# Kernel optimization log

Hardware: AMD Instinct MI355X
Metric: run time of the kernel (lower is better)

Reference implementation:

```python
import jax, jax.numpy as jnp
import numpy as np

B, S, D, H = 2, 2048, 1024, 16


def setup_inputs() -> dict:
    key = jax.random.key(0)
    kq, kk, kv1, kv2 = jax.random.split(key, 4)
    return {
        "q": jax.random.normal(kq, (B, S, D), dtype=jnp.float32),
        "k": jax.random.normal(kk, (B, S, D), dtype=jnp.float32),
        "v1": jax.random.normal(kv1, (B, S, D), dtype=jnp.float32),
        "v2": jax.random.normal(kv2, (B, S, D), dtype=jnp.float32),
        "num_attn_heads": 16,
    }


def _split_heads(x, h):
    b, s, d = x.shape
    return x.reshape(b, s, h, d // h).transpose(0, 2, 1, 3)  # [B,H,S,dh]


def reference(q, k, v1, v2, num_attn_heads):
    h = num_attn_heads
    b, s, d = q.shape
    dh = d // h
    qh = _split_heads(q, h)
    kh = _split_heads(k, h)
    v1h = _split_heads(v1, h)
    v2h = _split_heads(v2, h)
    scores = jnp.einsum("bhqd,bhkd->bhqk", qh, kh) / jnp.sqrt(jnp.float32(dh))
    # Faithful to create_mask(input, 0): nopeek = triu(ones, k=0); mask = (nopeek == 0)
    # -> only STRICTLY lower triangle is visible; diagonal and above get -1e9.
    # Row 0 is fully masked -> softmax uniform (same as torch behavior).
    allowed = jnp.tril(jnp.ones((s, s), dtype=bool), k=-1)  # [S,S] j < i
    scores = jnp.where(allowed[None, None], scores, jnp.float32(-1e9))
    p_attn = jax.nn.softmax(scores, axis=-1)  # dropout p=0.0 -> identity
    o1 = jnp.einsum("bhqk,bhkd->bhqd", p_attn, v1h)
    o2 = jnp.einsum("bhqk,bhkd->bhqd", p_attn, v2h)
    o1 = o1.transpose(0, 2, 1, 3).reshape(b, s, d)
    o2 = o2.transpose(0, 2, 1, 3).reshape(b, s, d)
    return (o1, o2)
```

## Files before the change

### kernel.cpp

```cpp
#include <hip/hip_runtime.h>

#define B_ 2
#define S_ 2048
#define D_ 1024
#define H_ 16
#define DH 64
#define OFF2 (B_ * S_ * D_)

typedef __attribute__((ext_vector_type(8))) __bf16 bf16x8;
typedef __attribute__((ext_vector_type(4))) float f32x4;
typedef __attribute__((ext_vector_type(4))) unsigned int u32x4;
typedef __attribute__((address_space(3))) unsigned int lds_u32;
typedef __attribute__((address_space(1))) const unsigned int glob_u32;

__device__ __forceinline__ unsigned short f2bf(float f) {
    return __builtin_bit_cast(unsigned short, (__bf16)f);
}
__device__ __forceinline__ float bf2f(unsigned short h) {
    unsigned int u = ((unsigned int)h) << 16;
    return __builtin_bit_cast(float, u);
}

template <int CTRL>
__device__ __forceinline__ float dpp_ror(float x) {
    return __builtin_bit_cast(float, __builtin_amdgcn_update_dpp(
        0, __builtin_bit_cast(int, x), CTRL, 0xf, 0xf, false));
}
__device__ __forceinline__ float rowsum16(float x) {
    x += dpp_ror<0x121>(x);
    x += dpp_ror<0x122>(x);
    x += dpp_ror<0x124>(x);
    x += dpp_ror<0x128>(x);
    return x;
}

__global__ void prep_all(const float* __restrict__ q, const float* __restrict__ k,
                         const float* __restrict__ v1, const float* __restrict__ v2,
                         unsigned short* __restrict__ qb, unsigned short* __restrict__ kb,
                         unsigned short* __restrict__ v1t, unsigned short* __restrict__ v2t) {
    int id = blockIdx.x;
    if (id < 4096) {
        int ysel = id & 1;
        int cid = (id >> 1) * 256 + threadIdx.x;
        const float* src = ysel ? k : q;
        unsigned short* dst = ysel ? kb : qb;
        float scale = ysel ? 1.0f : 0.125f * 1.4426950408889634f;
        int d8 = cid & 7;
        int s  = (cid >> 3) & (S_ - 1);
        int h  = (cid >> 14) & (H_ - 1);
        int b  = cid >> 18;
        int off = (b * S_ + s) * D_ + h * DH + d8 * 8;
        float4 f0 = *(const float4*)(src + off);
        float4 f1 = *(const float4*)(src + off + 4);
        unsigned int w0 = f2bf(f0.x * scale) | ((unsigned int)f2bf(f0.y * scale) << 16);
        unsigned int w1 = f2bf(f0.z * scale) | ((unsigned int)f2bf(f0.w * scale) << 16);
        unsigned int w2 = f2bf(f1.x * scale) | ((unsigned int)f2bf(f1.y * scale) << 16);
        unsigned int w3 = f2bf(f1.z * scale) | ((unsigned int)f2bf(f1.w * scale) << 16);
        u32x4 wv = {w0, w1, w2, w3};
        *(u32x4*)(dst + cid * 8) = wv;
        return;
    }
    __shared__ __align__(16) unsigned short ldsT[64][72];
    int id2 = id - 4096;
    int t = threadIdx.x;
    int s0 = (id2 & 31) * 64;
    int bh = (id2 >> 5) & 31;
    int b = bh >> 4, h = bh & 15;
    const float* src = (id2 >> 10) ? v2 : v1;
    unsigned short* dst = (id2 >> 10) ? v2t : v1t;
    {
        int sl = t >> 2, dc = t & 3;
        int off = (b * S_ + s0 + sl) * D_ + h * DH + dc * 16;
#pragma unroll
        for (int i4 = 0; i4 < 4; i4++) {
            float4 f = *(const float4*)(src + off + i4 * 4);
            int d = dc * 16 + i4 * 4;
            ldsT[d + 0][sl] = f2bf(f.x);
            ldsT[d + 1][sl] = f2bf(f.y);
            ldsT[d + 2][sl] = f2bf(f.z);
            ldsT[d + 3][sl] = f2bf(f.w);
        }
    }
    __syncthreads();
    {
        int d = t >> 2, sc = t & 3;
        u32x4 a = *(const u32x4*)(&ldsT[d][sc * 16]);
        u32x4 c = *(const u32x4*)(&ldsT[d][sc * 16 + 8]);
        int off = (bh * DH + d) * S_ + s0 + sc * 16;
        *(u32x4*)(dst + off) = a;
        *(u32x4*)(dst + off + 8) = c;
    }
}

__global__ __launch_bounds__(256) void flash_attn(
        const unsigned short* __restrict__ qb, const unsigned short* __restrict__ kb,
        const unsigned short* __restrict__ v1t, const unsigned short* __restrict__ v2t,
        float* __restrict__ out) {
    __shared__ __align__(16) unsigned short sK0[4096], sK1[4096];
    __shared__ __align__(16) unsigned short sV1[4096], sV2[4096];
    __shared__ __align__(16) unsigned short sP[4][1024];

    int tid = threadIdx.x;
    int w = tid >> 6, lane = tid & 63;
    int lr = lane & 15, lg = lane >> 4;

    int id = blockIdx.x;
    int xcd = id & 7;
    int j = id >> 3;
    int bh = xcd * 4 + (j & 3);
    int qt = 31 - (j >> 2);

    const unsigned short* gK  = kb  + bh * (S_ * DH);
    const unsigned short* gV1 = v1t + bh * (DH * S_);
    const unsigned short* gV2 = v2t + bh * (DH * S_);
    unsigned short* sPw = sP[w];

    int srow = tid >> 3, sco = tid & 7;

    auto stageV = [&](int t) {
#pragma unroll
        for (int jj = 0; jj < 2; jj++) {
            int row = srow + jj * 32;
            int cosw = (sco ^ (row & 7)) * 8;
            int c8 = (tid + jj * 256) * 8;
            __builtin_amdgcn_global_load_lds((glob_u32*)(gV1 + row * S_ + t * 64 + cosw),
                                             (lds_u32*)(sV1 + c8), 16, 0, 0);
            __builtin_amdgcn_global_load_lds((glob_u32*)(gV2 + row * S_ + t * 64 + cosw),
                                             (lds_u32*)(sV2 + c8), 16, 0, 0);
        }
    };
    auto stageK = [&](unsigned short* dK, int t) {
#pragma unroll
        for (int jj = 0; jj < 2; jj++) {
            int row = srow + jj * 32;
            int cosw = (sco ^ (row & 7)) * 8;
            int c8 = (tid + jj * 256) * 8;
            __builtin_amdgcn_global_load_lds((glob_u32*)(gK + (t * 64 + row) * 64 + cosw),
                                             (lds_u32*)(dK + c8), 16, 0, 0);
        }
    };

    bf16x8 qa[2];
    {
        int qoff = (bh * S_ + qt * 64 + w * 16 + lr) * DH + lg * 8;
        qa[0] = __builtin_bit_cast(bf16x8, *(const u32x4*)(qb + qoff));
        qa[1] = __builtin_bit_cast(bf16x8, *(const u32x4*)(qb + qoff + 32));
    }

    f32x4 acc1[4], acc2[4];
    float l[4];
#pragma unroll
    for (int dt = 0; dt < 4; dt++) {
        acc1[dt] = (f32x4){0.f, 0.f, 0.f, 0.f};
        acc2[dt] = (f32x4){0.f, 0.f, 0.f, 0.f};
    }
#pragma unroll
    for (int r = 0; r < 4; r++) l[r] = 0.f;

    stageK(sK0, 0);
    asm volatile("s_waitcnt vmcnt(0)" ::: "memory");
    __builtin_amdgcn_s_barrier();

    for (int t = 0; t <= qt; t++) {
        const unsigned short* cK = (t & 1) ? sK1 : sK0;
        unsigned short* nK       = (t & 1) ? sK0 : sK1;
        stageV(t);
        int tn = (t < qt) ? (t + 1) : qt;
        stageK(nK, tn);
        f32x4 s[4];
        __builtin_amdgcn_s_setprio(1);
#pragma unroll
        for (int n = 0; n < 4; n++) {
            f32x4 accs = (f32x4){0.f, 0.f, 0.f, 0.f};
#pragma unroll
            for (int ks = 0; ks < 2; ks++) {
                int kv = n * 16 + lr;
                int idx = ((kv << 6) + ks * 32 + lg * 8) ^ ((kv & 7) << 3);
                bf16x8 bk = __builtin_bit_cast(bf16x8, *(const u32x4*)(cK + idx));
                accs = __builtin_amdgcn_mfma_f32_16x16x32_bf16(qa[ks], bk, accs, 0, 0, 0);
            }
            s[n] = accs;
        }
        __builtin_amdgcn_s_setprio(0);
        if (t == qt) {
#pragma unroll
            for (int n = 0; n < 4; n++) {
                int kv = n * 16 + lr;
#pragma unroll
                for (int r = 0; r < 4; r++) {
                    int qrow = w * 16 + lg * 4 + r;
                    if (kv >= qrow) s[n][r] = -1e30f;
                }
            }
        }
#pragma unroll
        for (int n = 0; n < 4; n++)
#pragma unroll
            for (int r = 0; r < 4; r++) {
                float pv = __builtin_amdgcn_exp2f(s[n][r] - 20.0f);
                l[r] += pv;
                int rowp = lg * 4 + r, col = n * 16 + lr;
                sPw[((rowp << 6) + col) ^ ((rowp & 7) << 3)] = f2bf(pv);
            }
        asm volatile("s_waitcnt lgkmcnt(0)" ::: "memory");
        asm volatile("s_waitcnt vmcnt(2)" ::: "memory");
        __builtin_amdgcn_s_barrier();
        __builtin_amdgcn_s_setprio(1);
#pragma unroll
        for (int ks = 0; ks < 2; ks++) {
            int pidx = ((lr << 6) + ks * 32 + lg * 8) ^ ((lr & 7) << 3);
            bf16x8 ap = __builtin_bit_cast(bf16x8, *(const u32x4*)(sPw + pidx));
#pragma unroll
            for (int dt = 0; dt < 4; dt++) {
                int d = dt * 16 + lr;
                int vidx = ((d << 6) + ks * 32 + lg * 8) ^ ((d & 7) << 3);
                bf16x8 bv1 = __builtin_bit_cast(bf16x8, *(const u32x4*)(sV1 + vidx));
                acc1[dt] = __builtin_amdgcn_mfma_f32_16x16x32_bf16(ap, bv1, acc1[dt], 0, 0, 0);
                bf16x8 bv2 = __builtin_bit_cast(bf16x8, *(const u32x4*)(sV2 + vidx));
                acc2[dt] = __builtin_amdgcn_mfma_f32_16x16x32_bf16(ap, bv2, acc2[dt], 0, 0, 0);
            }
        }
        __builtin_amdgcn_s_setprio(0);
        asm volatile("s_waitcnt vmcnt(0)" ::: "memory");
        __builtin_amdgcn_s_barrier();
    }

    {
        int b = bh >> 4, h = bh & 15;
#pragma unroll
        for (int r = 0; r < 4; r++) {
            float lsum = rowsum16(l[r]);
            float inv = 1.0f / lsum;
            int qrow = qt * 64 + w * 16 + lg * 4 + r;
            int base = (b * S_ + qrow) * D_ + h * DH + lr;
#pragma unroll
            for (int dt = 0; dt < 4; dt++) {
                out[base + dt * 16] = acc1[dt][r] * inv;
                out[base + dt * 16 + OFF2] = acc2[dt][r] * inv;
            }
        }
    }
}

__global__ void row0_mean(const unsigned short* __restrict__ v1t,
                          const unsigned short* __restrict__ v2t,
                          float* __restrict__ out) {
    int wid = blockIdx.x * 4 + (threadIdx.x >> 6);
    int lane = threadIdx.x & 63;
    int tz = wid >> 11;
    int bhd = wid & 2047;
    const unsigned short* src = (tz ? v2t : v1t) + bhd * S_;
    float sum = 0.f;
#pragma unroll
    for (int kk = 0; kk < 4; kk++) {
        u32x4 v = *(const u32x4*)(src + (kk * 64 + lane) * 8);
#pragma unroll
        for (int jj = 0; jj < 4; jj++) {
            unsigned int u = v[jj];
            sum += bf2f((unsigned short)(u & 0xffff)) + bf2f((unsigned short)(u >> 16));
        }
    }
#pragma unroll
    for (int msk = 32; msk >= 1; msk >>= 1) sum += __shfl_xor(sum, msk, 64);
    if (lane == 0) {
        int b = bhd >> 10, rem = bhd & 1023, h = rem >> 6, d = rem & 63;
        out[tz * OFF2 + b * (S_ * D_) + h * DH + d] = sum * (1.0f / S_);
    }
}

extern "C" void kernel_launch(void* const* d_in, const int* in_sizes, int n_in,
                              void* d_out, int out_size, void* d_ws, size_t ws_size,
                              hipStream_t stream) {
    const float* q  = (const float*)d_in[0];
    const float* k  = (const float*)d_in[1];
    const float* v1 = (const float*)d_in[2];
    const float* v2 = (const float*)d_in[3];
    float* out = (float*)d_out;

    const int ELEMS = B_ * H_ * S_ * DH;
    unsigned short* qb  = (unsigned short*)d_ws;
    unsigned short* kb  = qb + ELEMS;
    unsigned short* v1t = kb + ELEMS;
    unsigned short* v2t = v1t + ELEMS;

    prep_all<<<6144, 256, 0, stream>>>(q, k, v1, v2, qb, kb, v1t, v2t);
    flash_attn<<<1024, 256, 0, stream>>>(qb, kb, v1t, v2t, out);
    row0_mean<<<1024, 256, 0, stream>>>(v1t, v2t, out);
}
```

Measured before the change: 76.63 us.

## Split PV matmul across waves by output tensor and row half via shared P tile

P is now written to a single block-wide shared tile instead of per-wave tiles. Each wave computes PV for one value tensor (V1 or V2) over 32 query rows, rather than both tensors over its own 16 rows. The end-of-iteration wait and barrier move to the start of the next iteration so the next tile's loads overlap more with compute. Row sums are reduced through LDS so each wave can normalize rows it did not compute. The intent is to halve V fragment LDS reads per wave and to remove a barrier per iteration, at the cost of extra P reads and tighter vmcnt accounting.

```diff
diff --git a/kernel.cpp b/kernel.cpp
--- a/kernel.cpp
+++ b/kernel.cpp
@@ -98,7 +98,7 @@
         float* __restrict__ out) {
     __shared__ __align__(16) unsigned short sK0[4096], sK1[4096];
     __shared__ __align__(16) unsigned short sV1[4096], sV2[4096];
-    __shared__ __align__(16) unsigned short sP[4][1024];
+    __shared__ __align__(16) unsigned short sP[4096];
 
     int tid = threadIdx.x;
     int w = tid >> 6, lane = tid & 63;
@@ -113,7 +113,6 @@
     const unsigned short* gK  = kb  + bh * (S_ * DH);
     const unsigned short* gV1 = v1t + bh * (DH * S_);
     const unsigned short* gV2 = v2t + bh * (DH * S_);
-    unsigned short* sPw = sP[w];
 
     int srow = tid >> 3, sco = tid & 7;
 
@@ -147,26 +146,27 @@
         qa[1] = __builtin_bit_cast(bf16x8, *(const u32x4*)(qb + qoff + 32));
     }
 
-    f32x4 acc1[4], acc2[4];
+    int tz = w >> 1, half = w & 1;
+    const unsigned short* cV = tz ? sV2 : sV1;
+
+    f32x4 acc[2][4];
     float l[4];
 #pragma unroll
-    for (int dt = 0; dt < 4; dt++) {
-        acc1[dt] = (f32x4){0.f, 0.f, 0.f, 0.f};
-        acc2[dt] = (f32x4){0.f, 0.f, 0.f, 0.f};
-    }
+    for (int m = 0; m < 2; m++)
+#pragma unroll
+        for (int dt = 0; dt < 4; dt++) acc[m][dt] = (f32x4){0.f, 0.f, 0.f, 0.f};
 #pragma unroll
     for (int r = 0; r < 4; r++) l[r] = 0.f;
 
     stageK(sK0, 0);
-    asm volatile("s_waitcnt vmcnt(0)" ::: "memory");
-    __builtin_amdgcn_s_barrier();
 
     for (int t = 0; t <= qt; t++) {
         const unsigned short* cK = (t & 1) ? sK1 : sK0;
         unsigned short* nK       = (t & 1) ? sK0 : sK1;
+        __builtin_amdgcn_s_barrier();
         stageV(t);
-        int tn = (t < qt) ? (t + 1) : qt;
-        stageK(nK, tn);
+        stageK(nK, (t < qt) ? t + 1 : qt);
+        asm volatile("s_waitcnt vmcnt(6)" ::: "memory");
         f32x4 s[4];
         __builtin_amdgcn_s_setprio(1);
 #pragma unroll
@@ -199,46 +199,56 @@
             for (int r = 0; r < 4; r++) {
                 float pv = __builtin_amdgcn_exp2f(s[n][r] - 20.0f);
                 l[r] += pv;
-                int rowp = lg * 4 + r, col = n * 16 + lr;
-                sPw[((rowp << 6) + col) ^ ((rowp & 7) << 3)] = f2bf(pv);
+                int row = w * 16 + lg * 4 + r, col = n * 16 + lr;
+                sP[((row << 6) + col) ^ ((row & 7) << 3)] = f2bf(pv);
             }
         asm volatile("s_waitcnt lgkmcnt(0)" ::: "memory");
         asm volatile("s_waitcnt vmcnt(2)" ::: "memory");
         __builtin_amdgcn_s_barrier();
         __builtin_amdgcn_s_setprio(1);
 #pragma unroll
-        for (int ks = 0; ks < 2; ks++) {
-            int pidx = ((lr << 6) + ks * 32 + lg * 8) ^ ((lr & 7) << 3);
-            bf16x8 ap = __builtin_bit_cast(bf16x8, *(const u32x4*)(sPw + pidx));
-#pragma unroll
-            for (int dt = 0; dt < 4; dt++) {
-                int d = dt * 16 + lr;
-                int vidx = ((d << 6) + ks * 32 + lg * 8) ^ ((d & 7) << 3);
-                bf16x8 bv1 = __builtin_bit_cast(bf16x8, *(const u32x4*)(sV1 + vidx));
-                acc1[dt] = __builtin_amdgcn_mfma_f32_16x16x32_bf16(ap, bv1, acc1[dt], 0, 0, 0);
-                bf16x8 bv2 = __builtin_bit_cast(bf16x8, *(const u32x4*)(sV2 + vidx));
-                acc2[dt] = __builtin_amdgcn_mfma_f32_16x16x32_bf16(ap, bv2, acc2[dt], 0, 0, 0);
-            }
-        }
+        for (int ks = 0; ks < 2; ks++)
+#pragma unroll
+            for (int m = 0; m < 2; m++) {
+                int row = half * 32 + m * 16 + lr;
+                int pidx = ((row << 6) + ks * 32 + lg * 8) ^ ((row & 7) << 3);
+                bf16x8 ap = __builtin_bit_cast(bf16x8, *(const u32x4*)(sP + pidx));
+#pragma unroll
+                for (int dt = 0; dt < 4; dt++) {
+                    int d = dt * 16 + lr;
+                    int vidx = ((d << 6) + ks * 32 + lg * 8) ^ ((d & 7) << 3);
+                    bf16x8 bv = __builtin_bit_cast(bf16x8, *(const u32x4*)(cV + vidx));
+                    acc[m][dt] = __builtin_amdgcn_mfma_f32_16x16x32_bf16(ap, bv, acc[m][dt], 0, 0, 0);
+                }
+            }
         __builtin_amdgcn_s_setprio(0);
-        asm volatile("s_waitcnt vmcnt(0)" ::: "memory");
-        __builtin_amdgcn_s_barrier();
-    }
+    }
+
+    asm volatile("s_waitcnt vmcnt(0)" ::: "memory");
+    __builtin_amdgcn_s_barrier();
+    float* lsh = (float*)sK0;
+#pragma unroll
+    for (int r = 0; r < 4; r++) {
+        float ls = rowsum16(l[r]);
+        if (lr == 0) lsh[w * 16 + lg * 4 + r] = ls;
+    }
+    asm volatile("s_waitcnt lgkmcnt(0)" ::: "memory");
+    __builtin_amdgcn_s_barrier();
 
     {
         int b = bh >> 4, h = bh & 15;
 #pragma unroll
-        for (int r = 0; r < 4; r++) {
-            float lsum = rowsum16(l[r]);
-            float inv = 1.0f / lsum;
-            int qrow = qt * 64 + w * 16 + lg * 4 + r;
-            int base = (b * S_ + qrow) * D_ + h * DH + lr;
-#pragma unroll
-            for (int dt = 0; dt < 4; dt++) {
-                out[base + dt * 16] = acc1[dt][r] * inv;
-                out[base + dt * 16 + OFF2] = acc2[dt][r] * inv;
-            }
-        }
+        for (int m = 0; m < 2; m++)
+#pragma unroll
+            for (int r = 0; r < 4; r++) {
+                int row = half * 32 + m * 16 + lg * 4 + r;
+                float inv = 1.0f / lsh[row];
+                int qrow = qt * 64 + row;
+                int base = (b * S_ + qrow) * D_ + h * DH + lr + tz * OFF2;
+#pragma unroll
+                for (int dt = 0; dt < 4; dt++)
+                    out[base + dt * 16] = acc[m][dt][r] * inv;
+            }
     }
 }
 
```

Result: faster. 74.23 us (-3.1%).

## Keep P in registers via transposed MFMA and permlane swaps, drop LDS P buffer

Applied to the files above, without the earlier changes.

Computes S transposed (K as A operand, Q as B operand) with the -20 softmax offset folded into the accumulator init. The P tile is then rearranged into the PV MFMA operand layout in registers with permlane32/permlane16 swaps instead of a round trip through LDS. The loop now has a single barrier at the top, with partial vmcnt waits in place of a full drain plus a second barrier. Outputs are written as float4 vectors with a simpler shuffle row-sum. The risks are correctness of the permlane mapping and of the relaxed synchronisation around buffer reuse.

```diff
diff --git a/kernel.cpp b/kernel.cpp
--- a/kernel.cpp
+++ b/kernel.cpp
@@ -6,32 +6,24 @@
 #define H_ 16
 #define DH 64
 #define OFF2 (B_ * S_ * D_)
+#define ELEMS (B_ * H_ * S_ * DH)
 
 typedef __attribute__((ext_vector_type(8))) __bf16 bf16x8;
 typedef __attribute__((ext_vector_type(4))) float f32x4;
 typedef __attribute__((ext_vector_type(4))) unsigned int u32x4;
+typedef __attribute__((ext_vector_type(2))) unsigned int u32x2;
 typedef __attribute__((address_space(3))) unsigned int lds_u32;
 typedef __attribute__((address_space(1))) const unsigned int glob_u32;
 
 __device__ __forceinline__ unsigned short f2bf(float f) {
     return __builtin_bit_cast(unsigned short, (__bf16)f);
+}
+__device__ __forceinline__ unsigned int pk2(float a, float b) {
+    return (unsigned int)f2bf(a) | ((unsigned int)f2bf(b) << 16);
 }
 __device__ __forceinline__ float bf2f(unsigned short h) {
     unsigned int u = ((unsigned int)h) << 16;
     return __builtin_bit_cast(float, u);
-}
-
-template <int CTRL>
-__device__ __forceinline__ float dpp_ror(float x) {
-    return __builtin_bit_cast(float, __builtin_amdgcn_update_dpp(
-        0, __builtin_bit_cast(int, x), CTRL, 0xf, 0xf, false));
-}
-__device__ __forceinline__ float rowsum16(float x) {
-    x += dpp_ror<0x121>(x);
-    x += dpp_ror<0x122>(x);
-    x += dpp_ror<0x124>(x);
-    x += dpp_ror<0x128>(x);
-    return x;
 }
 
 __global__ void prep_all(const float* __restrict__ q, const float* __restrict__ k,
@@ -52,11 +44,8 @@
         int off = (b * S_ + s) * D_ + h * DH + d8 * 8;
         float4 f0 = *(const float4*)(src + off);
         float4 f1 = *(const float4*)(src + off + 4);
-        unsigned int w0 = f2bf(f0.x * scale) | ((unsigned int)f2bf(f0.y * scale) << 16);
-        unsigned int w1 = f2bf(f0.z * scale) | ((unsigned int)f2bf(f0.w * scale) << 16);
-        unsigned int w2 = f2bf(f1.x * scale) | ((unsigned int)f2bf(f1.y * scale) << 16);
-        unsigned int w3 = f2bf(f1.z * scale) | ((unsigned int)f2bf(f1.w * scale) << 16);
-        u32x4 wv = {w0, w1, w2, w3};
+        u32x4 wv = {pk2(f0.x * scale, f0.y * scale), pk2(f0.z * scale, f0.w * scale),
+                    pk2(f1.x * scale, f1.y * scale), pk2(f1.z * scale, f1.w * scale)};
         *(u32x4*)(dst + cid * 8) = wv;
         return;
     }
@@ -98,24 +87,22 @@
         float* __restrict__ out) {
     __shared__ __align__(16) unsigned short sK0[4096], sK1[4096];
     __shared__ __align__(16) unsigned short sV1[4096], sV2[4096];
-    __shared__ __align__(16) unsigned short sP[4][1024];
 
     int tid = threadIdx.x;
     int w = tid >> 6, lane = tid & 63;
     int lr = lane & 15, lg = lane >> 4;
+    int srow = tid >> 3, sco = tid & 7;
 
     int id = blockIdx.x;
     int xcd = id & 7;
     int j = id >> 3;
     int bh = xcd * 4 + (j & 3);
     int qt = 31 - (j >> 2);
+    int b = bh >> 4, hh = bh & 15;
 
     const unsigned short* gK  = kb  + bh * (S_ * DH);
     const unsigned short* gV1 = v1t + bh * (DH * S_);
     const unsigned short* gV2 = v2t + bh * (DH * S_);
-    unsigned short* sPw = sP[w];
-
-    int srow = tid >> 3, sco = tid & 7;
 
     auto stageV = [&](int t) {
 #pragma unroll
@@ -148,96 +135,97 @@
     }
 
     f32x4 acc1[4], acc2[4];
-    float l[4];
 #pragma unroll
     for (int dt = 0; dt < 4; dt++) {
         acc1[dt] = (f32x4){0.f, 0.f, 0.f, 0.f};
         acc2[dt] = (f32x4){0.f, 0.f, 0.f, 0.f};
     }
-#pragma unroll
-    for (int r = 0; r < 4; r++) l[r] = 0.f;
+    float l = 0.f;
 
     stageK(sK0, 0);
-    asm volatile("s_waitcnt vmcnt(0)" ::: "memory");
-    __builtin_amdgcn_s_barrier();
 
     for (int t = 0; t <= qt; t++) {
         const unsigned short* cK = (t & 1) ? sK1 : sK0;
         unsigned short* nK       = (t & 1) ? sK0 : sK1;
+        __builtin_amdgcn_s_barrier();
         stageV(t);
-        int tn = (t < qt) ? (t + 1) : qt;
-        stageK(nK, tn);
+        stageK(nK, (t < qt) ? t + 1 : qt);
+        asm volatile("s_waitcnt vmcnt(6)" ::: "memory");
         f32x4 s[4];
         __builtin_amdgcn_s_setprio(1);
 #pragma unroll
         for (int n = 0; n < 4; n++) {
-            f32x4 accs = (f32x4){0.f, 0.f, 0.f, 0.f};
-#pragma unroll
-            for (int ks = 0; ks < 2; ks++) {
-                int kv = n * 16 + lr;
-                int idx = ((kv << 6) + ks * 32 + lg * 8) ^ ((kv & 7) << 3);
-                bf16x8 bk = __builtin_bit_cast(bf16x8, *(const u32x4*)(cK + idx));
-                accs = __builtin_amdgcn_mfma_f32_16x16x32_bf16(qa[ks], bk, accs, 0, 0, 0);
-            }
-            s[n] = accs;
+            int kv = n * 16 + lr;
+            int ix0 = ((kv << 6) + lg * 8) ^ ((kv & 7) << 3);
+            int ix1 = ((kv << 6) + 32 + lg * 8) ^ ((kv & 7) << 3);
+            bf16x8 k0 = __builtin_bit_cast(bf16x8, *(const u32x4*)(cK + ix0));
+            bf16x8 k1 = __builtin_bit_cast(bf16x8, *(const u32x4*)(cK + ix1));
+            f32x4 a = __builtin_amdgcn_mfma_f32_16x16x32_bf16(
+                k0, qa[0], (f32x4){-20.f, -20.f, -20.f, -20.f}, 0, 0, 0);
+            s[n] = __builtin_amdgcn_mfma_f32_16x16x32_bf16(k1, qa[1], a, 0, 0, 0);
         }
         __builtin_amdgcn_s_setprio(0);
         if (t == qt) {
 #pragma unroll
-            for (int n = 0; n < 4; n++) {
-                int kv = n * 16 + lr;
-#pragma unroll
-                for (int r = 0; r < 4; r++) {
-                    int qrow = w * 16 + lg * 4 + r;
-                    if (kv >= qrow) s[n][r] = -1e30f;
-                }
+            for (int n = 0; n < 4; n++)
+#pragma unroll
+                for (int r = 0; r < 4; r++)
+                    if (n * 16 + lg * 4 + r >= w * 16 + lr) s[n][r] = -1e30f;
+        }
+        u32x4 pa[2];
+#pragma unroll
+        for (int ks = 0; ks < 2; ks++) {
+            float p0[4], p1[4];
+#pragma unroll
+            for (int r = 0; r < 4; r++) {
+                p0[r] = __builtin_amdgcn_exp2f(s[2 * ks][r]);
+                p1[r] = __builtin_amdgcn_exp2f(s[2 * ks + 1][r]);
+                l += p0[r] + p1[r];
             }
-        }
-#pragma unroll
-        for (int n = 0; n < 4; n++)
-#pragma unroll
-            for (int r = 0; r < 4; r++) {
-                float pv = __builtin_amdgcn_exp2f(s[n][r] - 20.0f);
-                l[r] += pv;
-                int rowp = lg * 4 + r, col = n * 16 + lr;
-                sPw[((rowp << 6) + col) ^ ((rowp & 7) << 3)] = f2bf(pv);
-            }
-        asm volatile("s_waitcnt lgkmcnt(0)" ::: "memory");
+            unsigned int u0 = pk2(p0[0], p0[1]);
+            unsigned int u1 = pk2(p0[2], p0[3]);
+            unsigned int u2 = pk2(p1[0], p1[1]);
+            unsigned int u3 = pk2(p1[2], p1[3]);
+            u32x2 ab = __builtin_amdgcn_permlane32_swap(u0, u2, false, false);
+            u32x2 cd = __builtin_amdgcn_permlane32_swap(u1, u3, false, false);
+            u32x2 ab2 = __builtin_amdgcn_permlane16_swap(ab[0], ab[1], false, false);
+            u32x2 cd2 = __builtin_amdgcn_permlane16_swap(cd[0], cd[1], false, false);
+            pa[ks] = (u32x4){ab2[0], cd2[0], ab2[1], cd2[1]};
+        }
         asm volatile("s_waitcnt vmcnt(2)" ::: "memory");
         __builtin_amdgcn_s_barrier();
         __builtin_amdgcn_s_setprio(1);
 #pragma unroll
         for (int ks = 0; ks < 2; ks++) {
-            int pidx = ((lr << 6) + ks * 32 + lg * 8) ^ ((lr & 7) << 3);
-            bf16x8 ap = __builtin_bit_cast(bf16x8, *(const u32x4*)(sPw + pidx));
+            bf16x8 pab = __builtin_bit_cast(bf16x8, pa[ks]);
 #pragma unroll
             for (int dt = 0; dt < 4; dt++) {
                 int d = dt * 16 + lr;
-                int vidx = ((d << 6) + ks * 32 + lg * 8) ^ ((d & 7) << 3);
-                bf16x8 bv1 = __builtin_bit_cast(bf16x8, *(const u32x4*)(sV1 + vidx));
-                acc1[dt] = __builtin_amdgcn_mfma_f32_16x16x32_bf16(ap, bv1, acc1[dt], 0, 0, 0);
-                bf16x8 bv2 = __builtin_bit_cast(bf16x8, *(const u32x4*)(sV2 + vidx));
-                acc2[dt] = __builtin_amdgcn_mfma_f32_16x16x32_bf16(ap, bv2, acc2[dt], 0, 0, 0);
+                int vix = ((d << 6) + ks * 32 + lg * 8) ^ ((d & 7) << 3);
+                bf16x8 vf1 = __builtin_bit_cast(bf16x8, *(const u32x4*)(sV1 + vix));
+                acc1[dt] = __builtin_amdgcn_mfma_f32_16x16x32_bf16(vf1, pab, acc1[dt], 0, 0, 0);
+                bf16x8 vf2 = __builtin_bit_cast(bf16x8, *(const u32x4*)(sV2 + vix));
+                acc2[dt] = __builtin_amdgcn_mfma_f32_16x16x32_bf16(vf2, pab, acc2[dt], 0, 0, 0);
             }
         }
         __builtin_amdgcn_s_setprio(0);
-        asm volatile("s_waitcnt vmcnt(0)" ::: "memory");
-        __builtin_amdgcn_s_barrier();
-    }
-
-    {
-        int b = bh >> 4, h = bh & 15;
-#pragma unroll
-        for (int r = 0; r < 4; r++) {
-            float lsum = rowsum16(l[r]);
-            float inv = 1.0f / lsum;
-            int qrow = qt * 64 + w * 16 + lg * 4 + r;
-            int base = (b * S_ + qrow) * D_ + h * DH + lr;
-#pragma unroll
-            for (int dt = 0; dt < 4; dt++) {
-                out[base + dt * 16] = acc1[dt][r] * inv;
-                out[base + dt * 16 + OFF2] = acc2[dt][r] * inv;
-            }
+    }
+
+    asm volatile("s_waitcnt vmcnt(0)" ::: "memory");
+
+    float lt = l;
+    lt += __shfl_xor(lt, 16, 64);
+    lt += __shfl_xor(lt, 32, 64);
+    float inv = 1.0f / lt;
+    {
+        int qrow = qt * 64 + w * 16 + lr;
+        int base = (b * S_ + qrow) * D_ + hh * DH + lg * 4;
+#pragma unroll
+        for (int dt = 0; dt < 4; dt++) {
+            f32x4 o1 = acc1[dt] * inv;
+            f32x4 o2 = acc2[dt] * inv;
+            *(f32x4*)(out + base + dt * 16) = o1;
+            *(f32x4*)(out + base + dt * 16 + OFF2) = o2;
         }
     }
 }
@@ -277,7 +265,6 @@
     const float* v2 = (const float*)d_in[3];
     float* out = (float*)d_out;
 
-    const int ELEMS = B_ * H_ * S_ * DH;
     unsigned short* qb  = (unsigned short*)d_ws;
     unsigned short* kb  = qb + ELEMS;
     unsigned short* v1t = kb + ELEMS;
```

New measurement: 70.70 us. 7.7% less time.
